# Kernel optimization log

Hardware: AMD Instinct MI355X
Metric: run time of the kernel (lower is better)

## Reference

```python
import jax, jax.numpy as jnp
import numpy as np

EPS = 1e-5


def bin_act(x):
    # forward of Binaryactivation: sign (STE backward handled in fwdbwd module)
    return jnp.sign(x)


def bin_conv(x, w, stride, padding):
    # per-output-filter scaling factor = mean |w| over (in, kh, kw), detached
    scale = jax.lax.stop_gradient(jnp.mean(jnp.abs(w), axis=(1, 2, 3), keepdims=True))
    bw = scale * jnp.sign(w)
    rw = jnp.clip(w, -1.0, 1.0)
    # STE blend: forward uses binary weight, backward flows through clamp(w)
    filt = jax.lax.stop_gradient(bw - rw) + rw
    return jax.lax.conv_general_dilated(
        x, filt, window_strides=(stride, stride),
        padding=[(padding, padding), (padding, padding)],
        dimension_numbers=("NCHW", "OIHW", "NCHW"))


def batchnorm(x, gamma, beta):
    # training-mode BN: biased batch stats over (N, H, W)
    mean = jnp.mean(x, axis=(0, 2, 3), keepdims=True)
    var = jnp.mean((x - mean) ** 2, axis=(0, 2, 3), keepdims=True)
    xn = (x - mean) * jax.lax.rsqrt(var + EPS)
    return xn * gamma[None, :, None, None] + beta[None, :, None, None]


def prelu(x, a):
    a = a[None, :, None, None]
    return jnp.where(x >= 0, x, a * x)


def addbias(x, b):
    return x + b[None, :, None, None]


def setup_inputs() -> dict:
    key = jax.random.key(0)
    ks = jax.random.split(key, 4)
    C = 256
    x = jax.random.normal(ks[0], (32, C, 56, 56), dtype=jnp.float32)
    # BinaryConv weights init: uniform[0, 0.001)
    w3x3 = jax.random.uniform(ks[1], (C, C, 3, 3), dtype=jnp.float32) * 0.001
    wres = jax.random.uniform(ks[2], (C, C, 1, 1), dtype=jnp.float32) * 0.001
    zeros = jnp.zeros((C,), dtype=jnp.float32)
    ones = jnp.ones((C,), dtype=jnp.float32)
    prelu_init = jnp.full((C,), 0.25, dtype=jnp.float32)
    return {
        "x": x,
        "b1_1": zeros, "w3x3": w3x3, "bn1_g": ones, "bn1_b": zeros,
        "b1_2": zeros, "prelu1_a": prelu_init, "b1_3": zeros,
        "b2_1": zeros, "wres": wres, "bn2_g": ones, "bn2_b": zeros,
        "b2_2": zeros, "prelu2_a": prelu_init, "b2_3": zeros,
    }


def reference(x, b1_1, w3x3, bn1_g, bn1_b, b1_2, prelu1_a, b1_3,
              b2_1, wres, bn2_g, bn2_b, b2_2, prelu2_a, b2_3):
    # branch 1: bias -> sign -> binary 3x3 conv -> BN -> residual add
    x1 = bin_act(addbias(x, b1_1))
    x1 = bin_conv(x1, w3x3, stride=1, padding=1)
    x1 = batchnorm(x1, bn1_g, bn1_b)
    x = x + x1
    x = addbias(x, b1_2)
    x = prelu(x, prelu1_a)
    x = addbias(x, b1_3)
    # branch 2 (in_channel == out_channel): binary 1x1 conv residual
    x2 = bin_act(addbias(x, b2_1))
    x2 = bin_conv(x2, wres, stride=1, padding=0)
    x2 = batchnorm(x2, bn2_g, bn2_b)
    x2 = x2 + x
    x2 = addbias(x2, b2_2)
    x2 = prelu(x2, prelu2_a)
    x2 = addbias(x2, b2_3)
    return x2
```

## Files before the change

kernel.cpp:

```cpp
#include <hip/hip_runtime.h>
#include <cstdint>
#include <math.h>

#define HW    3136
#define NPIX  100352
#define NELEM 25690112

#define OFF_PW1   0u
#define OFF_PW2   73728u
#define OFF_CORR  81920u
#define OFF_SC1   86016u
#define OFF_SC2   87040u
#define OFF_A1    88064u
#define OFF_B1    89088u
#define OFF_A2    90112u
#define OFF_B2    91136u
#define OFF_ST    92160u
#define ST_BYTES  524288u
#define OFF_P1    616448u
#define OFF_P2    3827712u
#define OFF_S1    7038976u
#define OFF_S2    58419200u

__global__ void prep_w_k(const float* __restrict__ w3, const float* __restrict__ wr,
                         uint32_t* __restrict__ pw1, uint32_t* __restrict__ pw2,
                         float* __restrict__ sc1, float* __restrict__ sc2,
                         short* __restrict__ corrG) {
  const int o = blockIdx.x, l = threadIdx.x;
  const float* wo = w3 + (size_t)o * 2304;
  float s = 0.f;
  for (int i = l; i < 2304; i += 64) s += fabsf(wo[i]);
  for (int m = 32; m; m >>= 1) s += __shfl_xor(s, m, 64);
  if (l == 0) sc1[o] = s / 2304.0f;
  int wsum[9];
  for (int tap = 0; tap < 9; ++tap) {
    int cnt = 0;
    for (int jp = 0; jp < 4; ++jp) {
      float wv = wo[(size_t)(jp * 64 + l) * 9 + tap];
      unsigned long long m = __ballot(wv >= 0.0f);
      cnt += __popcll(m);
      if (l == 0) {
        pw1[(size_t)(o * 9 + tap) * 8 + jp * 2 + 0] = (uint32_t)m;
        pw1[(size_t)(o * 9 + tap) * 8 + jp * 2 + 1] = (uint32_t)(m >> 32);
      }
    }
    wsum[tap] = 2 * cnt - 256;
  }
  if (l == 0) {
    corrG[o * 8 + 0] = (short)(wsum[0] + wsum[1] + wsum[2]);
    corrG[o * 8 + 1] = (short)(wsum[6] + wsum[7] + wsum[8]);
    corrG[o * 8 + 2] = (short)(wsum[0] + wsum[3] + wsum[6]);
    corrG[o * 8 + 3] = (short)(wsum[2] + wsum[5] + wsum[8]);
    corrG[o * 8 + 4] = (short)wsum[0];
    corrG[o * 8 + 5] = (short)wsum[2];
    corrG[o * 8 + 6] = (short)wsum[6];
    corrG[o * 8 + 7] = (short)wsum[8];
  }
  const float* wro = wr + (size_t)o * 256;
  float s2 = 0.f;
  for (int i = l; i < 256; i += 64) s2 += fabsf(wro[i]);
  for (int m = 32; m; m >>= 1) s2 += __shfl_xor(s2, m, 64);
  if (l == 0) sc2[o] = s2 / 256.0f;
  for (int jp = 0; jp < 4; ++jp) {
    unsigned long long m = __ballot(wro[jp * 64 + l] >= 0.0f);
    if (l == 0) {
      pw2[(size_t)o * 8 + jp * 2 + 0] = (uint32_t)m;
      pw2[(size_t)o * 8 + jp * 2 + 1] = (uint32_t)(m >> 32);
    }
  }
}

__global__ __launch_bounds__(256) void pack1_k(const float* __restrict__ x,
                                               const float* __restrict__ b1_1,
                                               uint32_t* __restrict__ p1) {
  const int j = blockIdx.y;
  const int gpx = blockIdx.x * 256 + threadIdx.x;
  const int n = gpx / 784;
  const int p4 = (gpx - n * 784) * 4;
  const float* xb = x + ((size_t)n * 256 + j * 32) * HW + p4;
  uint32_t w0 = 0, w1 = 0, w2 = 0, w3 = 0;
#pragma unroll
  for (int cc = 0; cc < 32; ++cc) {
    float4 v = *(const float4*)(xb + (size_t)cc * HW);
    float bb = b1_1[j * 32 + cc];
    w0 |= (v.x + bb >= 0.f) ? (1u << cc) : 0u;
    w1 |= (v.y + bb >= 0.f) ? (1u << cc) : 0u;
    w2 |= (v.z + bb >= 0.f) ? (1u << cc) : 0u;
    w3 |= (v.w + bb >= 0.f) ? (1u << cc) : 0u;
  }
  uint4 o = {w0, w1, w2, w3};
  *(uint4*)&p1[(size_t)j * NPIX + gpx * 4] = o;
}

__global__ __launch_bounds__(256, 4) void conv1_k(const uint32_t* __restrict__ p1,
    const uint32_t* __restrict__ pw1, const short* __restrict__ corrG,
    short* __restrict__ S1, unsigned long long* __restrict__ st1) {
  __shared__ __align__(16) uint32_t actS[840];
  __shared__ __align__(16) uint32_t wtS[9728];
  __shared__ __align__(16) short    corrS[1024];
  const int tid = threadIdx.x;
  const int bx = blockIdx.x;
  const int ty = bx / 7, tx = bx % 7;
  const int n = blockIdx.y;
  const int zh = blockIdx.z;
  const int h0 = ty * 8 - 1, w0 = tx * 8 - 1;
  for (int i = tid; i < 800; i += 256) {
    int r = i / 80, cq = i % 80;
    int c = cq >> 3;
    int hh = h0 + r, ww = w0 + c;
    uint32_t v = 0;
    if ((unsigned)hh < 56u && (unsigned)ww < 56u)
      v = p1[(size_t)(cq & 7) * NPIX + (size_t)n * HW + hh * 56 + ww];
    actS[r * 84 + cq] = v;
  }
  const uint32_t* pwB = pw1 + (size_t)zh * 9216;
  for (int i = tid; i < 2304; i += 256) {
    int ch = i / 18, t4 = (i % 18) * 4;
    *(uint4*)&wtS[ch * 76 + t4] = *(const uint4*)(pwB + ch * 72 + t4);
  }
  if (tid < 128)
    ((uint4*)corrS)[tid] = ((const uint4*)(corrG + zh * 1024))[tid];
  __syncthreads();

  const int pr = tid & 7;
  const int chg = tid >> 3;
  const uint32_t* wp = wtS + chg * 76;

  int acc[4][8];
#pragma unroll
  for (int j = 0; j < 4; ++j)
#pragma unroll
    for (int k = 0; k < 8; ++k) acc[j][k] = 0;

#pragma unroll 1
  for (int dh = 0; dh < 3; ++dh) {
#pragma unroll 1
    for (int q4 = 0; q4 < 2; ++q4) {
      uint4 a10[10];
      const uint32_t* ar = actS + (pr + dh) * 84 + q4 * 4;
#pragma unroll
      for (int c2 = 0; c2 < 10; ++c2) a10[c2] = *(const uint4*)(ar + c2 * 8);
#pragma unroll
      for (int j = 0; j < 4; ++j) {
        const uint32_t* wj = wp + j * 2432 + q4 * 4 + dh * 24;
        uint4 wA = *(const uint4*)(wj + 0);
        uint4 wB = *(const uint4*)(wj + 8);
        uint4 wC = *(const uint4*)(wj + 16);
#pragma unroll
        for (int k = 0; k < 8; ++k) {
          uint4 a0 = a10[k];
          uint4 a1 = a10[k + 1];
          uint4 a2 = a10[k + 2];
          int t = acc[j][k];
          t += __builtin_popcount(a0.x ^ wA.x);
          t += __builtin_popcount(a0.y ^ wA.y);
          t += __builtin_popcount(a0.z ^ wA.z);
          t += __builtin_popcount(a0.w ^ wA.w);
          t += __builtin_popcount(a1.x ^ wB.x);
          t += __builtin_popcount(a1.y ^ wB.y);
          t += __builtin_popcount(a1.z ^ wB.z);
          t += __builtin_popcount(a1.w ^ wB.w);
          t += __builtin_popcount(a2.x ^ wC.x);
          t += __builtin_popcount(a2.y ^ wC.y);
          t += __builtin_popcount(a2.z ^ wC.z);
          t += __builtin_popcount(a2.w ^ wC.w);
          acc[j][k] = t;
        }
      }
    }
  }

  const int h = ty * 8 + pr;
  const bool hT = (h == 0), hB = (h == 55);
  const int slot = (bx + n * 49) & 63;
#pragma unroll
  for (int j = 0; j < 4; ++j) {
    const int ch_l = chg + 32 * j;
    const short* cw = &corrS[ch_l * 8];
    int cH = hT ? (int)cw[0] : (hB ? (int)cw[1] : 0);
    int s[8];
#pragma unroll
    for (int k = 0; k < 8; ++k) s[k] = 2304 - 2 * acc[j][k] + cH;
    if (tx == 0) s[0] += (int)cw[2] - (hT ? (int)cw[4] : (hB ? (int)cw[6] : 0));
    if (tx == 6) s[7] += (int)cw[3] - (hT ? (int)cw[5] : (hB ? (int)cw[7] : 0));
    int sm = 0, sq = 0;
#pragma unroll
    for (int k = 0; k < 8; ++k) { sm += s[k]; sq += s[k] * s[k]; }
    uint4 val;
    val.x = (uint32_t)(uint16_t)s[0] | ((uint32_t)(uint16_t)s[1] << 16);
    val.y = (uint32_t)(uint16_t)s[2] | ((uint32_t)(uint16_t)s[3] << 16);
    val.z = (uint32_t)(uint16_t)s[4] | ((uint32_t)(uint16_t)s[5] << 16);
    val.w = (uint32_t)(uint16_t)s[6] | ((uint32_t)(uint16_t)s[7] << 16);
    *(uint4*)&S1[(((size_t)n * 49 + bx) * 256 + zh * 128 + ch_l) * 64 + pr * 8] = val;
#pragma unroll
    for (int m = 1; m < 8; m <<= 1) { sm += __shfl_xor(sm, m, 64); sq += __shfl_xor(sq, m, 64); }
    if (pr == 0) {
      unsigned long long* st = st1 + ((size_t)(zh * 128 + ch_l) * 64 + slot) * 2;
      atomicAdd(&st[0], (unsigned long long)(long long)sm);
      atomicAdd(&st[1], (unsigned long long)(long long)sq);
    }
  }
}

__global__ void bnfin_k(const unsigned long long* __restrict__ st, const float* __restrict__ sc,
                        const float* __restrict__ g, const float* __restrict__ b,
                        float* __restrict__ A, float* __restrict__ B) {
  const int c = blockIdx.x, l = threadIdx.x;
  long long sm = (long long)st[((size_t)c * 64 + l) * 2 + 0];
  long long sq = (long long)st[((size_t)c * 64 + l) * 2 + 1];
  for (int m = 1; m < 64; m <<= 1) { sm += __shfl_xor(sm, m, 64); sq += __shfl_xor(sq, m, 64); }
  if (l == 0) {
    const double M = (double)NPIX;
    double mS = (double)sm / M;
    double vS = (double)sq / M - mS * mS;
    double scale = (double)sc[c];
    double mean = scale * mS;
    double var = scale * scale * vS;
    double rstd = 1.0 / sqrt(var + 1e-5);
    double gd = (double)g[c];
    A[c] = (float)(gd * scale * rstd);
    B[c] = (float)((double)b[c] - gd * mean * rstd);
  }
}

__global__ __launch_bounds__(256) void pack2_k(const float* __restrict__ x,
    const short* __restrict__ S1,
    const float* __restrict__ A1, const float* __restrict__ B1,
    const float* __restrict__ b1_2, const float* __restrict__ a1,
    const float* __restrict__ b1_3, const float* __restrict__ b2_1,
    uint32_t* __restrict__ p2) {
  const int j = blockIdx.y;
  const int gpx = blockIdx.x * 256 + threadIdx.x;
  const int n = gpx / 784;
  const int p4 = (gpx - n * 784) * 4;
  const int h = p4 / 56, w = p4 - (p4 / 56) * 56;
  const int tile = (h >> 3) * 7 + (w >> 3);
  const int px = (h & 7) * 8 + (w & 7);
  const float* xb = x + ((size_t)n * 256 + j * 32) * HW + p4;
  const short* s1b = S1 + (((size_t)n * 49 + tile) * 256 + j * 32) * 64 + px;
  uint32_t w0 = 0, w1 = 0, w2 = 0, w3 = 0;
#pragma unroll
  for (int cc = 0; cc < 32; ++cc) {
    int c = j * 32 + cc;
    float4 xv = *(const float4*)(xb + (size_t)cc * HW);
    short4 s1 = *(const short4*)(s1b + cc * 64);
    float Ac = A1[c], Bc = B1[c], p12 = b1_2[c], al = a1[c], p13 = b1_3[c], p21 = b2_1[c];
    float u, v, t;
    u = xv.x + (Ac * (float)s1.x + Bc) + p12; v = u >= 0.f ? u : al * u; t = v + p13 + p21;
    w0 |= (t >= 0.f) ? (1u << cc) : 0u;
    u = xv.y + (Ac * (float)s1.y + Bc) + p12; v = u >= 0.f ? u : al * u; t = v + p13 + p21;
    w1 |= (t >= 0.f) ? (1u << cc) : 0u;
    u = xv.z + (Ac * (float)s1.z + Bc) + p12; v = u >= 0.f ? u : al * u; t = v + p13 + p21;
    w2 |= (t >= 0.f) ? (1u << cc) : 0u;
    u = xv.w + (Ac * (float)s1.w + Bc) + p12; v = u >= 0.f ? u : al * u; t = v + p13 + p21;
    w3 |= (t >= 0.f) ? (1u << cc) : 0u;
  }
  uint4 o = {w0, w1, w2, w3};
  *(uint4*)&p2[(size_t)j * NPIX + gpx * 4] = o;
}

__global__ __launch_bounds__(256) void conv2_k(const uint32_t* __restrict__ p2,
                                               const uint32_t* __restrict__ pw2,
                                               short* __restrict__ S2,
                                               unsigned long long* __restrict__ st2) {
  __shared__ __align__(16) uint32_t actS[512];
  __shared__ __align__(16) uint32_t wtS[1024];
  const int tid = threadIdx.x;
  const int bx = blockIdx.x;
  const int zh = blockIdx.y;
  const int pg0 = bx * 64;
  for (int i = tid; i < 512; i += 256) {
    int gq = i >> 2, ws_ = i & 3;
    int pxl = gq >> 1, q4 = gq & 1;
    int q = q4 * 4 + ws_;
    actS[((gq ^ ((gq >> 3) & 15)) << 2) + ws_] = p2[q * NPIX + pg0 + pxl];
  }
  if (tid < 256)
    ((uint4*)wtS)[tid] = ((const uint4*)(pw2 + zh * 1024))[tid];
  __syncthreads();
  const int pxg = tid & 15, chg = tid >> 4;
  int acc[8][4];
#pragma unroll
  for (int j = 0; j < 8; ++j)
#pragma unroll
    for (int k = 0; k < 4; ++k) acc[j][k] = 0;
#pragma unroll
  for (int q4 = 0; q4 < 2; ++q4) {
    uint4 a[4];
#pragma unroll
    for (int k = 0; k < 4; ++k) {
      int gq = 8 * pxg + 2 * k + q4;
      a[k] = *(const uint4*)&actS[(gq ^ pxg) << 2];
    }
#pragma unroll
    for (int j = 0; j < 8; ++j) {
      uint4 w = *(const uint4*)&wtS[(chg + 16 * j) * 8 + q4 * 4];
#pragma unroll
      for (int k = 0; k < 4; ++k) {
        int t = acc[j][k];
        t += __builtin_popcount(a[k].x ^ w.x);
        t += __builtin_popcount(a[k].y ^ w.y);
        t += __builtin_popcount(a[k].z ^ w.z);
        t += __builtin_popcount(a[k].w ^ w.w);
        acc[j][k] = t;
      }
    }
  }
  const int slot = bx & 63;
#pragma unroll
  for (int j = 0; j < 8; ++j) {
    const int c_l = chg + 16 * j;
    int s[4], sm = 0, sq = 0;
#pragma unroll
    for (int k = 0; k < 4; ++k) {
      s[k] = 256 - 2 * acc[j][k];
      sm += s[k]; sq += s[k] * s[k];
    }
    short4 o4;
    o4.x = (short)s[0]; o4.y = (short)s[1]; o4.z = (short)s[2]; o4.w = (short)s[3];
    *(short4*)&S2[(((size_t)bx * 256) + zh * 128 + c_l) * 64 + pxg * 4] = o4;
#pragma unroll
    for (int m = 1; m < 16; m <<= 1) { sm += __shfl_xor(sm, m, 64); sq += __shfl_xor(sq, m, 64); }
    if (pxg == 0) {
      unsigned long long* st = st2 + ((size_t)(zh * 128 + c_l) * 64 + slot) * 2;
      atomicAdd(&st[0], (unsigned long long)(long long)sm);
      atomicAdd(&st[1], (unsigned long long)(long long)sq);
    }
  }
}

__global__ __launch_bounds__(256) void final_k(const float* __restrict__ x,
    const short* __restrict__ S1, const short* __restrict__ S2,
    const float* __restrict__ A1, const float* __restrict__ B1,
    const float* __restrict__ b1_2, const float* __restrict__ a1, const float* __restrict__ b1_3,
    const float* __restrict__ A2, const float* __restrict__ B2,
    const float* __restrict__ b2_2, const float* __restrict__ a2, const float* __restrict__ b2_3,
    float* __restrict__ out) {
  const int gi = blockIdx.x * 256 + threadIdx.x;
  const int i4 = gi * 4;
  const int nc = i4 / 3136;
  const int p = i4 - nc * 3136;
  const int n = nc >> 8, c = nc & 255;
  const int h = p / 56, w = p - (p / 56) * 56;
  const int tile = (h >> 3) * 7 + (w >> 3);
  const int px = (h & 7) * 8 + (w & 7);
  short4 s1 = *(const short4*)&S1[(((size_t)n * 49 + tile) * 256 + c) * 64 + px];
  const int pg = n * 3136 + p;
  short4 s2 = *(const short4*)&S2[((size_t)(pg >> 6) * 256 + c) * 64 + (pg & 63)];
  float4 xv = *(const float4*)&x[i4];
  const float A1c = A1[c], B1c = B1[c], P12 = b1_2[c], AL1 = a1[c], P13 = b1_3[c];
  const float A2c = A2[c], B2c = B2[c], P22 = b2_2[c], AL2 = a2[c], P23 = b2_3[c];
  float xs[4] = {xv.x, xv.y, xv.z, xv.w};
  float f1[4] = {(float)s1.x, (float)s1.y, (float)s1.z, (float)s1.w};
  float f2[4] = {(float)s2.x, (float)s2.y, (float)s2.z, (float)s2.w};
  float o[4];
#pragma unroll
  for (int e = 0; e < 4; ++e) {
    float u = xs[e] + (A1c * f1[e] + B1c);
    u = u + P12;
    float v = u >= 0.0f ? u : AL1 * u;
    float t = v + P13;
    float z = (A2c * f2[e] + B2c) + t;
    z = z + P22;
    float vv = z >= 0.0f ? z : AL2 * z;
    o[e] = vv + P23;
  }
  float4 ov = {o[0], o[1], o[2], o[3]};
  *(float4*)&out[i4] = ov;
}

extern "C" void kernel_launch(void* const* d_in, const int* in_sizes, int n_in,
                              void* d_out, int out_size, void* d_ws, size_t ws_size,
                              hipStream_t stream) {
  const float* x    = (const float*)d_in[0];
  const float* b1_1 = (const float*)d_in[1];
  const float* w3x3 = (const float*)d_in[2];
  const float* bn1g = (const float*)d_in[3];
  const float* bn1b = (const float*)d_in[4];
  const float* b1_2 = (const float*)d_in[5];
  const float* a1   = (const float*)d_in[6];
  const float* b1_3 = (const float*)d_in[7];
  const float* b2_1 = (const float*)d_in[8];
  const float* wres = (const float*)d_in[9];
  const float* bn2g = (const float*)d_in[10];
  const float* bn2b = (const float*)d_in[11];
  const float* b2_2 = (const float*)d_in[12];
  const float* a2   = (const float*)d_in[13];
  const float* b2_3 = (const float*)d_in[14];

  char* ws = (char*)d_ws;
  uint32_t* pw1 = (uint32_t*)(ws + OFF_PW1);
  uint32_t* pw2 = (uint32_t*)(ws + OFF_PW2);
  short* corrG = (short*)(ws + OFF_CORR);
  float* sc1 = (float*)(ws + OFF_SC1);
  float* sc2 = (float*)(ws + OFF_SC2);
  float* A1 = (float*)(ws + OFF_A1);
  float* B1 = (float*)(ws + OFF_B1);
  float* A2 = (float*)(ws + OFF_A2);
  float* B2 = (float*)(ws + OFF_B2);
  unsigned long long* st1 = (unsigned long long*)(ws + OFF_ST);
  unsigned long long* st2 = (unsigned long long*)(ws + OFF_ST + 262144u);
  uint32_t* p1 = (uint32_t*)(ws + OFF_P1);
  uint32_t* p2 = (uint32_t*)(ws + OFF_P2);
  short* S1 = (short*)(ws + OFF_S1);
  short* S2 = (short*)(ws + OFF_S2);

  hipMemsetAsync(ws + OFF_ST, 0, ST_BYTES, stream);
  prep_w_k<<<256, 64, 0, stream>>>(w3x3, wres, pw1, pw2, sc1, sc2, corrG);
  pack1_k<<<dim3(98, 8), 256, 0, stream>>>(x, b1_1, p1);
  conv1_k<<<dim3(49, 32, 2), 256, 0, stream>>>(p1, pw1, corrG, S1, st1);
  bnfin_k<<<256, 64, 0, stream>>>(st1, sc1, bn1g, bn1b, A1, B1);
  pack2_k<<<dim3(98, 8), 256, 0, stream>>>(x, S1, A1, B1, b1_2, a1, b1_3, b2_1, p2);
  conv2_k<<<dim3(1568, 2), 256, 0, stream>>>(p2, pw2, S2, st2);
  bnfin_k<<<256, 64, 0, stream>>>(st2, sc2, bn2g, bn2b, A2, B2);
  final_k<<<25088, 256, 0, stream>>>(x, S1, S2, A1, B1, b1_2, a1, b1_3,
                                     A2, B2, b2_2, a2, b2_3, (float*)d_out);
}
```

Before: 498.2 us.

## Widen weight prep to four waves and drop padded weight layout in conv1

The weight-prep kernel now uses 256 threads per output filter, so each thread loads its 9 taps contiguously, with shared-memory reduction of the sums and popcounts. In conv1 the padded 76-word weight row stride becomes an unpadded 72-word stride, which allows a flat vectorised copy and shrinks shared memory. The correction terms are read straight from global memory instead of being staged in LDS. The unpadded stride risks more LDS bank conflicts on the weight reads in the inner popcount loop.

```diff
diff --git a/kernel.cpp b/kernel.cpp
--- a/kernel.cpp
+++ b/kernel.cpp
@@ -22,31 +22,52 @@
 #define OFF_S1    7038976u
 #define OFF_S2    58419200u
 
-__global__ void prep_w_k(const float* __restrict__ w3, const float* __restrict__ wr,
+__global__ __launch_bounds__(256) void prep_w_k(const float* __restrict__ w3,
+                         const float* __restrict__ wr,
                          uint32_t* __restrict__ pw1, uint32_t* __restrict__ pw2,
                          float* __restrict__ sc1, float* __restrict__ sc2,
                          short* __restrict__ corrG) {
-  const int o = blockIdx.x, l = threadIdx.x;
-  const float* wo = w3 + (size_t)o * 2304;
+  __shared__ float s1S[4], s2S[4];
+  __shared__ int cntS[9][4];
+  const int o = blockIdx.x;
+  const int tid = threadIdx.x;
+  const int l = tid & 63, wv = tid >> 6;
+  const float* wo = w3 + (size_t)o * 2304 + (size_t)tid * 9;
+  float w9[9];
+#pragma unroll
+  for (int t = 0; t < 9; ++t) w9[t] = wo[t];
   float s = 0.f;
-  for (int i = l; i < 2304; i += 64) s += fabsf(wo[i]);
+#pragma unroll
+  for (int t = 0; t < 9; ++t) s += fabsf(w9[t]);
+#pragma unroll
   for (int m = 32; m; m >>= 1) s += __shfl_xor(s, m, 64);
-  if (l == 0) sc1[o] = s / 2304.0f;
-  int wsum[9];
-  for (int tap = 0; tap < 9; ++tap) {
-    int cnt = 0;
-    for (int jp = 0; jp < 4; ++jp) {
-      float wv = wo[(size_t)(jp * 64 + l) * 9 + tap];
-      unsigned long long m = __ballot(wv >= 0.0f);
-      cnt += __popcll(m);
-      if (l == 0) {
-        pw1[(size_t)(o * 9 + tap) * 8 + jp * 2 + 0] = (uint32_t)m;
-        pw1[(size_t)(o * 9 + tap) * 8 + jp * 2 + 1] = (uint32_t)(m >> 32);
-      }
-    }
-    wsum[tap] = 2 * cnt - 256;
-  }
+#pragma unroll
+  for (int t = 0; t < 9; ++t) {
+    unsigned long long mb = __ballot(w9[t] >= 0.0f);
+    if (l == 0) {
+      pw1[(size_t)(o * 9 + t) * 8 + wv * 2 + 0] = (uint32_t)mb;
+      pw1[(size_t)(o * 9 + t) * 8 + wv * 2 + 1] = (uint32_t)(mb >> 32);
+      cntS[t][wv] = __popcll(mb);
+    }
+  }
+  float v2 = wr[(size_t)o * 256 + tid];
+  float s2 = fabsf(v2);
+#pragma unroll
+  for (int m = 32; m; m >>= 1) s2 += __shfl_xor(s2, m, 64);
+  unsigned long long mb2 = __ballot(v2 >= 0.0f);
   if (l == 0) {
+    pw2[(size_t)o * 8 + wv * 2 + 0] = (uint32_t)mb2;
+    pw2[(size_t)o * 8 + wv * 2 + 1] = (uint32_t)(mb2 >> 32);
+    s1S[wv] = s; s2S[wv] = s2;
+  }
+  __syncthreads();
+  if (tid == 0) {
+    sc1[o] = (s1S[0] + s1S[1] + s1S[2] + s1S[3]) / 2304.0f;
+    sc2[o] = (s2S[0] + s2S[1] + s2S[2] + s2S[3]) / 256.0f;
+    int wsum[9];
+#pragma unroll
+    for (int t = 0; t < 9; ++t)
+      wsum[t] = 2 * (cntS[t][0] + cntS[t][1] + cntS[t][2] + cntS[t][3]) - 256;
     corrG[o * 8 + 0] = (short)(wsum[0] + wsum[1] + wsum[2]);
     corrG[o * 8 + 1] = (short)(wsum[6] + wsum[7] + wsum[8]);
     corrG[o * 8 + 2] = (short)(wsum[0] + wsum[3] + wsum[6]);
@@ -55,18 +76,6 @@
     corrG[o * 8 + 5] = (short)wsum[2];
     corrG[o * 8 + 6] = (short)wsum[6];
     corrG[o * 8 + 7] = (short)wsum[8];
-  }
-  const float* wro = wr + (size_t)o * 256;
-  float s2 = 0.f;
-  for (int i = l; i < 256; i += 64) s2 += fabsf(wro[i]);
-  for (int m = 32; m; m >>= 1) s2 += __shfl_xor(s2, m, 64);
-  if (l == 0) sc2[o] = s2 / 256.0f;
-  for (int jp = 0; jp < 4; ++jp) {
-    unsigned long long m = __ballot(wro[jp * 64 + l] >= 0.0f);
-    if (l == 0) {
-      pw2[(size_t)o * 8 + jp * 2 + 0] = (uint32_t)m;
-      pw2[(size_t)o * 8 + jp * 2 + 1] = (uint32_t)(m >> 32);
-    }
   }
 }
 
@@ -96,8 +105,7 @@
     const uint32_t* __restrict__ pw1, const short* __restrict__ corrG,
     short* __restrict__ S1, unsigned long long* __restrict__ st1) {
   __shared__ __align__(16) uint32_t actS[840];
-  __shared__ __align__(16) uint32_t wtS[9728];
-  __shared__ __align__(16) short    corrS[1024];
+  __shared__ __align__(16) uint32_t wtS[9216];
   const int tid = threadIdx.x;
   const int bx = blockIdx.x;
   const int ty = bx / 7, tx = bx % 7;
@@ -114,17 +122,13 @@
     actS[r * 84 + cq] = v;
   }
   const uint32_t* pwB = pw1 + (size_t)zh * 9216;
-  for (int i = tid; i < 2304; i += 256) {
-    int ch = i / 18, t4 = (i % 18) * 4;
-    *(uint4*)&wtS[ch * 76 + t4] = *(const uint4*)(pwB + ch * 72 + t4);
-  }
-  if (tid < 128)
-    ((uint4*)corrS)[tid] = ((const uint4*)(corrG + zh * 1024))[tid];
+  for (int i = tid; i < 2304; i += 256)
+    ((uint4*)wtS)[i] = ((const uint4*)pwB)[i];
   __syncthreads();
 
   const int pr = tid & 7;
   const int chg = tid >> 3;
-  const uint32_t* wp = wtS + chg * 76;
+  const uint32_t* wp = wtS + chg * 72;
 
   int acc[4][8];
 #pragma unroll
@@ -142,7 +146,7 @@
       for (int c2 = 0; c2 < 10; ++c2) a10[c2] = *(const uint4*)(ar + c2 * 8);
 #pragma unroll
       for (int j = 0; j < 4; ++j) {
-        const uint32_t* wj = wp + j * 2432 + q4 * 4 + dh * 24;
+        const uint32_t* wj = wp + j * 2304 + q4 * 4 + dh * 24;
         uint4 wA = *(const uint4*)(wj + 0);
         uint4 wB = *(const uint4*)(wj + 8);
         uint4 wC = *(const uint4*)(wj + 16);
@@ -176,13 +180,14 @@
 #pragma unroll
   for (int j = 0; j < 4; ++j) {
     const int ch_l = chg + 32 * j;
-    const short* cw = &corrS[ch_l * 8];
-    int cH = hT ? (int)cw[0] : (hB ? (int)cw[1] : 0);
+    short c8[8];
+    *(int4*)c8 = *(const int4*)(corrG + (size_t)(zh * 128 + ch_l) * 8);
+    int cH = hT ? (int)c8[0] : (hB ? (int)c8[1] : 0);
     int s[8];
 #pragma unroll
     for (int k = 0; k < 8; ++k) s[k] = 2304 - 2 * acc[j][k] + cH;
-    if (tx == 0) s[0] += (int)cw[2] - (hT ? (int)cw[4] : (hB ? (int)cw[6] : 0));
-    if (tx == 6) s[7] += (int)cw[3] - (hT ? (int)cw[5] : (hB ? (int)cw[7] : 0));
+    if (tx == 0) s[0] += (int)c8[2] - (hT ? (int)c8[4] : (hB ? (int)c8[6] : 0));
+    if (tx == 6) s[7] += (int)c8[3] - (hT ? (int)c8[5] : (hB ? (int)c8[7] : 0));
     int sm = 0, sq = 0;
 #pragma unroll
     for (int k = 0; k < 8; ++k) { sm += s[k]; sq += s[k] * s[k]; }
@@ -406,7 +411,7 @@
   short* S2 = (short*)(ws + OFF_S2);
 
   hipMemsetAsync(ws + OFF_ST, 0, ST_BYTES, stream);
-  prep_w_k<<<256, 64, 0, stream>>>(w3x3, wres, pw1, pw2, sc1, sc2, corrG);
+  prep_w_k<<<256, 256, 0, stream>>>(w3x3, wres, pw1, pw2, sc1, sc2, corrG);
   pack1_k<<<dim3(98, 8), 256, 0, stream>>>(x, b1_1, p1);
   conv1_k<<<dim3(49, 32, 2), 256, 0, stream>>>(p1, pw1, corrG, S1, st1);
   bnfin_k<<<256, 64, 0, stream>>>(st1, sc1, bn1g, bn1b, A1, B1);
```

Result: faster. 477.2 us (-4.2%).
